# Kernel optimization log

Measured on AMD Instinct MI355X. Metric: run time of the kernel, lower is better.

## Reference

```python
import jax, jax.numpy as jnp
import numpy as np

# ---- config (mirrors init_kwargs) ----
R = 0.15          # ball-query radius
K = 32            # neighbors per ball
SP_STRIDE = 32    # spatial FPS stride
T_KERNEL = 3      # temporal tube length (odd)
T_STRIDE = 2
T_PAD = (1, 1)    # replicate padding
C0, C1 = 64, 128  # mlp_planes


def setup_inputs() -> dict:
    key = jax.random.key(0)
    k1, k2, k3 = jax.random.split(key, 3)
    B, T, N = 4, 32, 4096
    xyzs = jax.random.uniform(k1, (B, T, N, 3), dtype=jnp.float32)
    # 1x1 conv weights (no bias, no BN): conv_d: 4 -> C0, mlp: C0 -> C1
    Wd = jax.random.normal(k2, (C0, 4), dtype=jnp.float32) * (1.0 / np.sqrt(4))
    Wm = jax.random.normal(k3, (C1, C0), dtype=jnp.float32) * (1.0 / np.sqrt(C0))
    return {"xyzs": xyzs, "Wd": Wd, "Wm": Wm}


def _fps(xyz, m):
    """Furthest point sampling. xyz: (G,N,3) -> (G,m) int32, first index = 0."""
    G, N, _ = xyz.shape
    def step(carry, _):
        dist, last = carry                                   # (G,N), (G,)
        p = jnp.take_along_axis(xyz, last[:, None, None], axis=1)  # (G,1,3)
        d = jnp.sum((xyz - p) ** 2, axis=-1)                 # (G,N)
        dist = jnp.minimum(dist, d)
        nxt = jnp.argmax(dist, axis=-1).astype(jnp.int32)
        return (dist, nxt), nxt
    init = (jnp.full((G, N), 1e10, dtype=xyz.dtype), jnp.zeros((G,), jnp.int32))
    _, nxts = jax.lax.scan(step, init, None, length=m - 1)   # (m-1, G)
    return jnp.concatenate([jnp.zeros((G, 1), jnp.int32), jnp.swapaxes(nxts, 0, 1)], axis=1)


def _ball_query(r, k, neighbor_xyz, anchor_xyz):
    """First-k-within-radius, invalid slots filled with first valid (PointNet++ semantics).
    neighbor: (G,N,3), anchor: (G,M,3) -> idx (G,M,k) int32."""
    N = neighbor_xyz.shape[1]
    d2 = jnp.sum((anchor_xyz[:, :, None, :] - neighbor_xyz[:, None, :, :]) ** 2, axis=-1)  # (G,M,N)
    score = jnp.where(d2 < r * r, jnp.arange(N, dtype=jnp.int32), N)
    neg_topk, _ = jax.lax.top_k(-score, k)   # k smallest scores (ascending point index)
    idx = -neg_topk                          # (G,M,k)
    first = idx[..., :1]
    first = jnp.where(first == N, 0, first)
    return jnp.where(idx == N, first, idx)


def _group(pts, idx):
    """pts: (G,N,C), idx: (G,M,k) -> (G,M,k,C)."""
    G, M, k = idx.shape
    flat = jnp.take_along_axis(pts, idx.reshape(G, M * k)[..., None], axis=1)
    return flat.reshape(G, M, k, pts.shape[-1])


def _forward(xyzs, Wd, Wm):
    B, T, N, _ = xyzs.shape
    # replicate temporal padding
    xyz_pad = jnp.concatenate([xyzs[:, :1]] * T_PAD[0] + [xyzs] + [xyzs[:, -1:]] * T_PAD[1], axis=1)
    Tp = T + T_PAD[0] + T_PAD[1]
    half = T_KERNEL // 2
    ts = half + T_STRIDE * np.arange((Tp - T_KERNEL) // T_STRIDE + 1)  # output frame centers
    F = len(ts)
    M = N // SP_STRIDE

    center = xyz_pad[:, ts].reshape(B * F, N, 3)          # (G,N,3)
    anchor_idx = _fps(center, M)                          # (G,M)
    anchor = jnp.take_along_axis(center, anchor_idx[..., None], axis=1)  # (G,M,3)

    feat_sum = None
    for dt in range(-half, half + 1):                     # temporal tube (len 3)
        neigh = xyz_pad[:, ts + dt].reshape(B * F, N, 3)
        idx = _ball_query(R, K, neigh, anchor)            # (G,M,K)
        grouped = _group(neigh, idx)                      # (G,M,K,3)
        disp = grouped - anchor[:, :, None, :]
        tchan = jnp.full(disp.shape[:-1] + (1,), float(dt), dtype=disp.dtype)
        d4 = jnp.concatenate([disp, tchan], axis=-1)      # (G,M,K,4)
        h = jax.nn.relu(jnp.einsum('gmkc,oc->gmko', d4, Wd))   # conv_d + ReLU
        h = jax.nn.relu(jnp.einsum('gmki,oi->gmko', h, Wm))    # mlp + ReLU
        feat = jnp.max(h, axis=2)                         # spatial max pool over K -> (G,M,C1)
        feat_sum = feat if feat_sum is None else feat_sum + feat  # temporal sum pool

    new_xyzs = anchor.reshape(B, F, M, 3)
    new_features = jnp.transpose(feat_sum.reshape(B, F, M, C1), (0, 1, 3, 2))  # (B,F,C1,M)
    return new_xyzs, new_features


def reference(xyzs, Wd, Wm):
    return _forward(xyzs, Wd, Wm)
```

## Files before the change

### kernel.cpp

```cpp
#include <hip/hip_runtime.h>
#include <stdint.h>

#define B_   4
#define T_   32
#define N_   4096
#define F_   16
#define G_   64
#define M_   128
#define K_   32
#define C0_  64
#define C1_  128

typedef short  short8 __attribute__((ext_vector_type(8)));
typedef float  f32x4  __attribute__((ext_vector_type(4)));

static __device__ __forceinline__ short f2bf(float x) {
    union { float f; unsigned u; } v; v.f = x;
    unsigned r = (v.u + 0x7FFFu + ((v.u >> 16) & 1u)) >> 16;
    return (short)r;
}
static __device__ __forceinline__ float bf2f(short h) {
    union { float f; unsigned u; } v; v.u = ((unsigned)(unsigned short)h) << 16;
    return v.f;
}

template<int CTRL>
static __device__ __forceinline__ unsigned long long dpp_u64(unsigned long long v) {
    int lo = __builtin_amdgcn_update_dpp(0, (int)(unsigned)v,         CTRL, 0xF, 0xF, false);
    int hi = __builtin_amdgcn_update_dpp(0, (int)(unsigned)(v >> 32), CTRL, 0xF, 0xF, false);
    return ((unsigned long long)(unsigned)hi << 32) | (unsigned)lo;
}

__global__ __launch_bounds__(256) void wsplit_kernel(const float* __restrict__ Wm,
                                                     short* __restrict__ Bhi_g,
                                                     short* __restrict__ Blo_g)
{
    int id = blockIdx.x * 256 + threadIdx.x;
    int o = id >> 3, c = id & 7;
    const float* wp = Wm + o * C0_ + c * 8;
    short8 hv, lv;
#pragma unroll
    for (int e = 0; e < 8; ++e) {
        float v = wp[e];
        short h = f2bf(v);
        short l = f2bf(v - bf2f(h));
        hv[e] = h; lv[e] = l;
    }
    int dst = o * C0_ + c * 8;
    *reinterpret_cast<short8*>(&Bhi_g[dst]) = hv;
    *reinterpret_cast<short8*>(&Blo_g[dst]) = lv;
}

__global__ __launch_bounds__(512) void fps_kernel(const float* __restrict__ xyzs,
                                                  float* __restrict__ anchors,
                                                  float* __restrict__ out_xyz)
{
#pragma clang fp contract(off)
    const int g = blockIdx.x;
    const int b = g >> 4, f = g & 15;
    const float* base = xyzs + ((size_t)(b * T_ + 2 * f) * N_) * 3;
    const int t = threadIdx.x;
    const int lane = t & 63;
    const int wid = t >> 6;

    __shared__ float cxs[N_], cys[N_], czs[N_];
    __shared__ unsigned long long sred[2][8];

    float x[8], y[8], z[8], dist[8];
#pragma unroll
    for (int j = 0; j < 8; ++j) {
        int p = j * 512 + t;
        float xx = base[p * 3 + 0];
        float yy = base[p * 3 + 1];
        float zz = base[p * 3 + 2];
        x[j] = xx; y[j] = yy; z[j] = zz; dist[j] = 1e10f;
        cxs[p] = xx; cys[p] = yy; czs[p] = zz;
    }

    float px = base[0], py = base[1], pz = base[2];
    float rx = 0.f, ry = 0.f, rz = 0.f;
    if (t == 0) { rx = px; ry = py; rz = pz; }
    __syncthreads();

    for (int it = 1; it < M_; ++it) {
        float bd = -1.0f; int bi = 0;
#pragma unroll
        for (int j = 0; j < 8; ++j) {
            float dx = x[j] - px;
            float dy = y[j] - py;
            float dz = z[j] - pz;
            float d = dx * dx + dy * dy;
            d = d + dz * dz;
            float nd = fminf(dist[j], d);
            dist[j] = nd;
            if (nd > bd) { bd = nd; bi = j * 512 + t; }
        }
        unsigned long long key =
            ((unsigned long long)__float_as_uint(bd) << 32) | (unsigned)(N_ - 1 - bi);
        unsigned long long k2;
        k2 = dpp_u64<0x111>(key); key = (k2 > key) ? k2 : key;
        k2 = dpp_u64<0x112>(key); key = (k2 > key) ? k2 : key;
        k2 = dpp_u64<0x114>(key); key = (k2 > key) ? k2 : key;
        k2 = dpp_u64<0x118>(key); key = (k2 > key) ? k2 : key;
        k2 = __shfl_xor(key, 16); key = (k2 > key) ? k2 : key;
        k2 = __shfl_xor(key, 32); key = (k2 > key) ? k2 : key;
        const int par = it & 1;
        if (lane == 63) sred[par][wid] = key;
        __syncthreads();
        unsigned long long ck = sred[par][0];
#pragma unroll
        for (int w = 1; w < 8; ++w) {
            unsigned long long ok = sred[par][w];
            ck = (ok > ck) ? ok : ck;
        }
        int ci = (N_ - 1) - (int)(ck & 0xFFFFFFFFu);
        px = cxs[ci]; py = cys[ci]; pz = czs[ci];
        if (t == it) { rx = px; ry = py; rz = pz; }
    }

    if (t < M_) {
        size_t ao = ((size_t)g * M_ + t) * 3;
        anchors[ao + 0] = rx; anchors[ao + 1] = ry; anchors[ao + 2] = rz;
        out_xyz[ao + 0] = rx; out_xyz[ao + 1] = ry; out_xyz[ao + 2] = rz;
    }
}

__global__ __launch_bounds__(256) void ballq_kernel(const float* __restrict__ xyzs,
                                                    const float* __restrict__ anchors,
                                                    int* __restrict__ widx)
{
#pragma clang fp contract(off)
    const float R2 = 0.0225f;
    const int wave = (blockIdx.x << 2) + (threadIdx.x >> 6);
    const int lane = threadIdx.x & 63;
    const int m   = wave % M_;
    const int gd  = wave / M_;
    const int dti = gd % 3;
    const int g   = gd / 3;
    const int b = g >> 4, f = g & 15;
    int tn = 2 * f + dti - 1;
    if (tn < 0) tn = 0;
    const float* nb = xyzs + ((size_t)(b * T_ + tn) * N_) * 3;
    const float* aw = anchors + ((size_t)g * M_ + m) * 3;
    const float ax = aw[0], ay = aw[1], az = aw[2];

    __shared__ int sbuf[4][K_];
    int* buf = sbuf[threadIdx.x >> 6];
    const unsigned long long lanebit = 1ULL << lane;

    int filled = 0;
    for (int cb = 0; cb < 8 && filled < K_; ++cb) {
        unsigned long long mk[8];
#pragma unroll
        for (int u = 0; u < 8; ++u) {
            int p = cb * 512 + u * 64 + lane;
            float dx = nb[p * 3 + 0] - ax;
            float dy = nb[p * 3 + 1] - ay;
            float dz = nb[p * 3 + 2] - az;
            float d2 = dx * dx + dy * dy;
            d2 = d2 + dz * dz;
            mk[u] = __ballot(d2 < R2);
        }
#pragma unroll
        for (int u = 0; u < 8; ++u) {
            if (mk[u] & lanebit) {
                int slot = filled + __popcll(mk[u] & (lanebit - 1ULL));
                if (slot < K_) buf[slot] = cb * 512 + u * 64 + lane;
            }
            filled += __popcll(mk[u]);
        }
    }
    __syncthreads();
    if (lane < K_) {
        int first = (filled > 0) ? buf[0] : 0;
        int v = (lane < filled) ? buf[lane] : first;
        widx[(size_t)wave * K_ + lane] = v;
    }
}

__global__ __launch_bounds__(256, 2) void mlp_kernel(const float* __restrict__ xyzs,
                                                     const float* __restrict__ Wd,
                                                     const short* __restrict__ Bhi_g,
                                                     const short* __restrict__ Blo_g,
                                                     const float* __restrict__ anchors,
                                                     const int* __restrict__ widx,
                                                     float* __restrict__ out_feat)
{
    const int t   = threadIdx.x;
    const int blk = blockIdx.x;
    const int g   = blk >> 6;
    const int m0  = (blk & 63) * 2;
    const int b = g >> 4, f = g & 15;

    const int lane = t & 63;
    const int w    = t >> 6;
    const int wml  = w & 1;
    const int wn   = w >> 1;
    const int row0 = lane & 15;
    const int kg   = lane >> 4;

    __shared__ __align__(16) short Ahi[192 * C0_];
    __shared__ float wd_s[C0_ * 4];
    __shared__ float pmf[2][C1_];

    short8 bh[4][2], bl[4][2];
#pragma unroll
    for (int nt = 0; nt < 4; ++nt) {
        int o = wn * 64 + nt * 16 + row0;
#pragma unroll
        for (int ks = 0; ks < 2; ++ks) {
            int off = o * C0_ + (ks * 4 + kg) * 8;
            bh[nt][ks] = *reinterpret_cast<const short8*>(&Bhi_g[off]);
            bl[nt][ks] = *reinterpret_cast<const short8*>(&Blo_g[off]);
        }
    }

    wd_s[t] = Wd[t];

    float dx = 0.f, dy = 0.f, dz = 0.f, dt4 = 0.f;
    if (t < 192) {
        int ml  = (t >= 96) ? 1 : 0;
        int rr  = t - ml * 96;
        int dti = rr >> 5, k = rr & 31;
        int m   = m0 + ml;
        int tn  = 2 * f + dti - 1;
        if (tn < 0) tn = 0;
        const float* nb = xyzs + ((size_t)(b * T_ + tn) * N_) * 3;
        int idx = widx[((size_t)(g * 3 + dti) * M_ + m) * K_ + k];
        const float* aw = anchors + ((size_t)g * M_ + m) * 3;
        dx = nb[idx * 3 + 0] - aw[0];
        dy = nb[idx * 3 + 1] - aw[1];
        dz = nb[idx * 3 + 2] - aw[2];
        dt4 = (float)(dti - 1);
    }
    __syncthreads();

    if (t < 192) {
#pragma unroll
        for (int u = 0; u < 8; ++u) {
            short8 hv;
#pragma unroll
            for (int e = 0; e < 8; ++e) {
                float4 wv = *reinterpret_cast<const float4*>(&wd_s[(u * 8 + e) * 4]);
                float s = dx * wv.x + dy * wv.y + dz * wv.z + dt4 * wv.w;
                hv[e] = f2bf(fmaxf(s, 0.0f));
            }
            *reinterpret_cast<short8*>(&Ahi[t * C0_ + ((u ^ (t & 7)) << 3)]) = hv;
        }
    }
    __syncthreads();

    f32x4 acc[6][4];
#pragma unroll
    for (int mt = 0; mt < 6; ++mt)
#pragma unroll
        for (int nt = 0; nt < 4; ++nt) {
            acc[mt][nt][0] = 0.f; acc[mt][nt][1] = 0.f;
            acc[mt][nt][2] = 0.f; acc[mt][nt][3] = 0.f;
        }

#pragma unroll
    for (int ks = 0; ks < 2; ++ks) {
        int chunk = ks * 4 + kg;
        short8 ah[6];
#pragma unroll
        for (int mt = 0; mt < 6; ++mt) {
            int r = wml * 96 + mt * 16 + row0;
            ah[mt] = *reinterpret_cast<const short8*>(&Ahi[r * C0_ + ((chunk ^ (r & 7)) << 3)]);
        }
#pragma unroll
        for (int mt = 0; mt < 6; ++mt)
#pragma unroll
            for (int nt = 0; nt < 4; ++nt) {
                acc[mt][nt] = __builtin_amdgcn_mfma_f32_16x16x32_bf16(ah[mt], bh[nt][ks], acc[mt][nt], 0, 0, 0);
                acc[mt][nt] = __builtin_amdgcn_mfma_f32_16x16x32_bf16(ah[mt], bl[nt][ks], acc[mt][nt], 0, 0, 0);
            }
    }

#pragma unroll
    for (int nt = 0; nt < 4; ++nt) {
        float fs = 0.f;
#pragma unroll
        for (int dti = 0; dti < 3; ++dti) {
            f32x4 a0 = acc[dti * 2 + 0][nt];
            f32x4 a1 = acc[dti * 2 + 1][nt];
            float mv = fmaxf(fmaxf(fmaxf(a0[0], a0[1]), fmaxf(a0[2], a0[3])),
                             fmaxf(fmaxf(a1[0], a1[1]), fmaxf(a1[2], a1[3])));
            mv = fmaxf(mv, 0.0f);
            mv = fmaxf(mv, __shfl_xor(mv, 16));
            mv = fmaxf(mv, __shfl_xor(mv, 32));
            fs += mv;
        }
        if (lane < 16) pmf[wml][wn * 64 + nt * 16 + lane] = fs;
    }
    __syncthreads();

    if (t < C1_) {
        float2 v = make_float2(pmf[0][t], pmf[1][t]);
        *reinterpret_cast<float2*>(&out_feat[((size_t)g * C1_ + t) * M_ + m0]) = v;
    }
}

extern "C" void kernel_launch(void* const* d_in, const int* in_sizes, int n_in,
                              void* d_out, int out_size, void* d_ws, size_t ws_size,
                              hipStream_t stream)
{
    (void)in_sizes; (void)n_in; (void)out_size; (void)ws_size;
    const float* xyzs = (const float*)d_in[0];
    const float* Wd   = (const float*)d_in[1];
    const float* Wm   = (const float*)d_in[2];
    float* out = (float*)d_out;

    char* ws = (char*)d_ws;
    short* Bhi_g   = (short*)ws;
    short* Blo_g   = (short*)(ws + 16384);
    float* anchors = (float*)(ws + 32768);
    int*   widx    = (int*)(ws + 32768 + (size_t)G_ * M_ * 3 * 4);

    float* out_xyz  = out;
    float* out_feat = out + G_ * M_ * 3;

    hipLaunchKernelGGL(wsplit_kernel, dim3(4),               dim3(256), 0, stream, Wm, Bhi_g, Blo_g);
    hipLaunchKernelGGL(fps_kernel,    dim3(G_),              dim3(512), 0, stream, xyzs, anchors, out_xyz);
    hipLaunchKernelGGL(ballq_kernel,  dim3(G_ * 3 * M_ / 4), dim3(256), 0, stream, xyzs, anchors, widx);
    hipLaunchKernelGGL(mlp_kernel,    dim3(G_ * 64),         dim3(256), 0, stream, xyzs, Wd, Bhi_g, Blo_g, anchors, widx, out_feat);
}
```

Before: 258.0 us.

## Fuse weight split into FPS and carry winner coordinates through reduction

Folds the weight bf16 hi/lo split kernel into the FPS launch as extra blocks, removing one kernel launch. FPS now uses 256 threads holding 16 points each, so the cross-wave reduction covers 4 waves instead of 8. The winning lane writes its point coordinates next to its key, so the LDS copy of all 4096 points and the indexed lookup after each barrier are gone. The cost is more registers per thread and more serial work per thread in each of the 127 iterations.

```diff
diff --git a/kernel.cpp b/kernel.cpp
--- a/kernel.cpp
+++ b/kernel.cpp
@@ -31,61 +31,59 @@
     return ((unsigned long long)(unsigned)hi << 32) | (unsigned)lo;
 }
 
-__global__ __launch_bounds__(256) void wsplit_kernel(const float* __restrict__ Wm,
-                                                     short* __restrict__ Bhi_g,
-                                                     short* __restrict__ Blo_g)
-{
-    int id = blockIdx.x * 256 + threadIdx.x;
-    int o = id >> 3, c = id & 7;
-    const float* wp = Wm + o * C0_ + c * 8;
-    short8 hv, lv;
-#pragma unroll
-    for (int e = 0; e < 8; ++e) {
-        float v = wp[e];
-        short h = f2bf(v);
-        short l = f2bf(v - bf2f(h));
-        hv[e] = h; lv[e] = l;
-    }
-    int dst = o * C0_ + c * 8;
-    *reinterpret_cast<short8*>(&Bhi_g[dst]) = hv;
-    *reinterpret_cast<short8*>(&Blo_g[dst]) = lv;
-}
-
-__global__ __launch_bounds__(512) void fps_kernel(const float* __restrict__ xyzs,
+__global__ __launch_bounds__(256) void fps_kernel(const float* __restrict__ xyzs,
                                                   float* __restrict__ anchors,
-                                                  float* __restrict__ out_xyz)
+                                                  float* __restrict__ out_xyz,
+                                                  const float* __restrict__ Wm,
+                                                  short* __restrict__ Bhi_g,
+                                                  short* __restrict__ Blo_g)
 {
 #pragma clang fp contract(off)
+    if (blockIdx.x >= G_) {
+        int id = (blockIdx.x - G_) * 256 + threadIdx.x;
+        int o = id >> 3, c = id & 7;
+        const float* wp = Wm + o * C0_ + c * 8;
+        short8 hv, lv;
+#pragma unroll
+        for (int e = 0; e < 8; ++e) {
+            float v = wp[e];
+            short h = f2bf(v);
+            short l = f2bf(v - bf2f(h));
+            hv[e] = h; lv[e] = l;
+        }
+        int dst = o * C0_ + c * 8;
+        *reinterpret_cast<short8*>(&Bhi_g[dst]) = hv;
+        *reinterpret_cast<short8*>(&Blo_g[dst]) = lv;
+        return;
+    }
+
     const int g = blockIdx.x;
     const int b = g >> 4, f = g & 15;
     const float* base = xyzs + ((size_t)(b * T_ + 2 * f) * N_) * 3;
     const int t = threadIdx.x;
-    const int lane = t & 63;
     const int wid = t >> 6;
 
-    __shared__ float cxs[N_], cys[N_], czs[N_];
-    __shared__ unsigned long long sred[2][8];
-
-    float x[8], y[8], z[8], dist[8];
-#pragma unroll
-    for (int j = 0; j < 8; ++j) {
-        int p = j * 512 + t;
-        float xx = base[p * 3 + 0];
-        float yy = base[p * 3 + 1];
-        float zz = base[p * 3 + 2];
-        x[j] = xx; y[j] = yy; z[j] = zz; dist[j] = 1e10f;
-        cxs[p] = xx; cys[p] = yy; czs[p] = zz;
+    __shared__ unsigned long long skey[2][4];
+    __shared__ float4 scrd[2][4];
+
+    float x[16], y[16], z[16], dist[16];
+#pragma unroll
+    for (int j = 0; j < 16; ++j) {
+        int p = j * 256 + t;
+        x[j] = base[p * 3 + 0];
+        y[j] = base[p * 3 + 1];
+        z[j] = base[p * 3 + 2];
+        dist[j] = 1e10f;
     }
 
     float px = base[0], py = base[1], pz = base[2];
     float rx = 0.f, ry = 0.f, rz = 0.f;
     if (t == 0) { rx = px; ry = py; rz = pz; }
-    __syncthreads();
 
     for (int it = 1; it < M_; ++it) {
         float bd = -1.0f; int bi = 0;
 #pragma unroll
-        for (int j = 0; j < 8; ++j) {
+        for (int j = 0; j < 16; ++j) {
             float dx = x[j] - px;
             float dy = y[j] - py;
             float dz = z[j] - pz;
@@ -93,28 +91,37 @@
             d = d + dz * dz;
             float nd = fminf(dist[j], d);
             dist[j] = nd;
-            if (nd > bd) { bd = nd; bi = j * 512 + t; }
-        }
-        unsigned long long key =
+            if (nd > bd) { bd = nd; bi = j * 256 + t; }
+        }
+        unsigned long long mykey =
             ((unsigned long long)__float_as_uint(bd) << 32) | (unsigned)(N_ - 1 - bi);
-        unsigned long long k2;
-        k2 = dpp_u64<0x111>(key); key = (k2 > key) ? k2 : key;
-        k2 = dpp_u64<0x112>(key); key = (k2 > key) ? k2 : key;
-        k2 = dpp_u64<0x114>(key); key = (k2 > key) ? k2 : key;
-        k2 = dpp_u64<0x118>(key); key = (k2 > key) ? k2 : key;
+        unsigned long long key = mykey, k2;
+        k2 = dpp_u64<0xB1>(key);  key = (k2 > key) ? k2 : key;
+        k2 = dpp_u64<0x4E>(key);  key = (k2 > key) ? k2 : key;
+        k2 = dpp_u64<0x124>(key); key = (k2 > key) ? k2 : key;
+        k2 = dpp_u64<0x128>(key); key = (k2 > key) ? k2 : key;
         k2 = __shfl_xor(key, 16); key = (k2 > key) ? k2 : key;
         k2 = __shfl_xor(key, 32); key = (k2 > key) ? k2 : key;
         const int par = it & 1;
-        if (lane == 63) sred[par][wid] = key;
+        if (mykey == key) {
+            float wx = x[0], wy = y[0], wz = z[0];
+#pragma unroll
+            for (int j = 1; j < 16; ++j) {
+                if (bi == j * 256 + t) { wx = x[j]; wy = y[j]; wz = z[j]; }
+            }
+            skey[par][wid] = key;
+            scrd[par][wid] = make_float4(wx, wy, wz, 0.f);
+        }
         __syncthreads();
-        unsigned long long ck = sred[par][0];
-#pragma unroll
-        for (int w = 1; w < 8; ++w) {
-            unsigned long long ok = sred[par][w];
-            ck = (ok > ck) ? ok : ck;
-        }
-        int ci = (N_ - 1) - (int)(ck & 0xFFFFFFFFu);
-        px = cxs[ci]; py = cys[ci]; pz = czs[ci];
+        unsigned long long ck = skey[par][0];
+        float4 cc = scrd[par][0];
+#pragma unroll
+        for (int w = 1; w < 4; ++w) {
+            unsigned long long ok = skey[par][w];
+            float4 oc = scrd[par][w];
+            if (ok > ck) { ck = ok; cc = oc; }
+        }
+        px = cc.x; py = cc.y; pz = cc.z;
         if (t == it) { rx = px; ry = py; rz = pz; }
     }
 
@@ -320,8 +327,9 @@
     float* out_xyz  = out;
     float* out_feat = out + G_ * M_ * 3;
 
-    hipLaunchKernelGGL(wsplit_kernel, dim3(4),               dim3(256), 0, stream, Wm, Bhi_g, Blo_g);
-    hipLaunchKernelGGL(fps_kernel,    dim3(G_),              dim3(512), 0, stream, xyzs, anchors, out_xyz);
-    hipLaunchKernelGGL(ballq_kernel,  dim3(G_ * 3 * M_ / 4), dim3(256), 0, stream, xyzs, anchors, widx);
-    hipLaunchKernelGGL(mlp_kernel,    dim3(G_ * 64),         dim3(256), 0, stream, xyzs, Wd, Bhi_g, Blo_g, anchors, widx, out_feat);
-}
+    hipLaunchKernelGGL(fps_kernel,    dim3(G_ + 4),           dim3(256), 0, stream,
+                       xyzs, anchors, out_xyz, Wm, Bhi_g, Blo_g);
+    hipLaunchKernelGGL(ballq_kernel,  dim3(G_ * 3 * M_ / 4),  dim3(256), 0, stream, xyzs, anchors, widx);
+    hipLaunchKernelGGL(mlp_kernel,    dim3(G_ * 64),          dim3(256), 0, stream,
+                       xyzs, Wd, Bhi_g, Blo_g, anchors, widx, out_feat);
+}
```

Result: slower. 316.4 us (+22.6%).
